# Optimization experiments

Hardware: AMD Instinct MI355X
Metric: run time of the kernel (lower is better)

## Reference

```python
import jax, jax.numpy as jnp
import numpy as np

HEADS = 8
HEIGHT = 512
WIDTH = 512
LATENT = 64  # height // 8
N_INST = 8


def setup_inputs() -> dict:
    key = jax.random.key(0)
    ks = jax.random.split(key, 8)
    C, Cx, L, N = 320, 768, 77, N_INST
    HW = LATENT * LATENT
    hidden_states = jax.random.normal(ks[0], (2, HW, C), jnp.float32)
    encoder_hidden_states = jax.random.normal(ks[1], (N + 3, L, Cx), jnp.float32)
    # non-degenerate normalized boxes (x0, y0, x1, y1)
    rng = np.random.default_rng(0)
    x0 = rng.uniform(0.0, 0.5, (N,)).astype(np.float32)
    y0 = rng.uniform(0.0, 0.5, (N,)).astype(np.float32)
    x1 = (x0 + rng.uniform(0.2, 0.45, (N,))).astype(np.float32)
    y1 = (y0 + rng.uniform(0.2, 0.45, (N,))).astype(np.float32)
    bboxes = jnp.asarray(np.stack([x0, y0, x1, y1], axis=-1)[None], jnp.float32)  # (1, N, 4)
    s = 0.02
    Wq = jax.random.normal(ks[2], (C, C), jnp.float32) * s
    Wk = jax.random.normal(ks[3], (Cx, C), jnp.float32) * s
    Wv = jax.random.normal(ks[4], (Cx, C), jnp.float32) * s
    Wo = jax.random.normal(ks[5], (C, C), jnp.float32) * s
    bo = jnp.zeros((C,), jnp.float32)
    return dict(hidden_states=hidden_states, encoder_hidden_states=encoder_hidden_states,
                bboxes=bboxes, Wq=Wq, Wk=Wk, Wv=Wv, Wo=Wo, bo=bo)


def _heads(x):
    # (B, S, H*D) -> (B*H, S, D)   [diffusers head_to_batch_dim]
    B, S, C = x.shape
    D = C // HEADS
    return x.reshape(B, S, HEADS, D).transpose(0, 2, 1, 3).reshape(B * HEADS, S, D)


def _unheads(x):
    # (B*H, S, D) -> (B, S, H*D)   [diffusers batch_to_head_dim]
    BH, S, D = x.shape
    B = BH // HEADS
    return x.reshape(B, HEADS, S, D).transpose(0, 2, 1, 3).reshape(B, S, HEADS * D)


def _forward(hidden_states, encoder_hidden_states, bboxes, Wq, Wk, Wv, Wo, bo):
    N = bboxes.shape[1]
    HW = hidden_states.shape[1]
    # drop the extra (MIGC) text embedding row, as in the processor
    ehs = encoder_hidden_states[:-1]  # (N+2, L, Cx)
    # batch = [uncond, cond repeated instance_num+1 times]
    hs = jnp.concatenate([hidden_states[:1],
                          jnp.repeat(hidden_states[1:2], N + 1, axis=0)], axis=0)  # (N+2, HW, C)
    q = _heads(hs @ Wq)
    k = _heads(ehs @ Wk)
    v = _heads(ehs @ Wv)
    scale = 1.0 / jnp.sqrt(jnp.asarray(q.shape[-1], q.dtype))
    probs = jax.nn.softmax(jnp.einsum('bqd,bkd->bqk', q, k) * scale, axis=-1)  # ((N+2)*H, HW, L)
    out = _unheads(jnp.einsum('bqk,bkd->bqd', probs, v))  # (N+2, HW, C)
    out = out @ Wo + bo
    hs_uncond = out[:1]
    cond_ca = out[1:][None]  # (1, N+1, HW, C)
    # rasterize per-instance bbox masks at full res (int() truncation == floor for positives)
    b = bboxes[0]  # (N, 4) = x0, y0, x1, y1
    w_min = jnp.floor(WIDTH * b[:, 0])[:, None, None]
    w_max = jnp.floor(WIDTH * b[:, 2])[:, None, None]
    h_min = jnp.floor(HEIGHT * b[:, 1])[:, None, None]
    h_max = jnp.floor(HEIGHT * b[:, 3])[:, None, None]
    rows = jnp.arange(HEIGHT, dtype=jnp.float32)[None, :, None]
    cols = jnp.arange(WIDTH, dtype=jnp.float32)[None, None, :]
    masks = ((rows >= h_min) & (rows < h_max) & (cols >= w_min) & (cols < w_max)).astype(jnp.float32)  # (N,H,W)
    gmask = jax.image.resize(masks, (N, LATENT, LATENT), method='bilinear')  # (N, 64, 64)
    # NaiveFuser: phase weights = [0.1 (full prompt), 10*mask_i], normalized sum over phases
    phase_w = jnp.concatenate([jnp.full((1, HW), 0.1, jnp.float32),
                               gmask.reshape(N, HW) * 10.0], axis=0)  # (N+1, HW)
    w = phase_w[None, :, :, None]  # (1, N+1, HW, 1)
    fused = (cond_ca * w).sum(axis=1) / (w.sum(axis=1) + 1e-6)  # (1, HW, C)
    return jnp.concatenate([hs_uncond, fused], axis=0)  # (2, HW, C)


def reference(hidden_states, encoder_hidden_states, bboxes, Wq, Wk, Wv, Wo, bo):
    return _forward(hidden_states, encoder_hidden_states, bboxes, Wq, Wk, Wv, Wo, bo)
```

## Files before the change

### kernel.cpp

```cpp
#include <hip/hip_runtime.h>
#include <math.h>

#define HW 4096
#define C 320
#define CX 768
#define L 77
#define NB 10
#define NH 8
#define HD 40
#define NINST 8
#define KVC 640
#define SCALE 0.15811388300841898f
#define PSTR 104
#define KSTR 48
#define VSTR 104

typedef _Float16 half8v __attribute__((ext_vector_type(8)));
typedef _Float16 half4v __attribute__((ext_vector_type(4)));
typedef float f32x4 __attribute__((ext_vector_type(4)));

#define KBH (80 * KSTR)
#define VBH (48 * VSTR)

#define SEG_MASK   16
#define N_CVT1     (2 * HW * C / 4)
#define N_CVT2     (NB * L * CX / 4)
#define SEG_CVT    (((N_CVT1 + N_CVT2) + 255) / 256)
#define SEG_WPACK  240
#define SEG_VTZ    195
#define SEG_KPAD   6
#define NPREP      (SEG_MASK + SEG_CVT + SEG_WPACK + SEG_VTZ + SEG_KPAD)

__device__ __forceinline__ float axis_profile(int o, float lo, float hi) {
    float num = 0.f, den = 0.f;
    int j0 = 8 * o - 4;
#pragma unroll
    for (int t = 0; t < 16; ++t) {
        int j = j0 + t;
        float wt = 1.0f - fabsf((float)t - 7.5f) * 0.125f;
        if (j >= 0 && j < 512) {
            den += wt;
            float fj = (float)j;
            if (fj >= lo && fj < hi) num += wt;
        }
    }
    return num / den;
}

__global__ __launch_bounds__(256) void prep_kernel(
        const float* __restrict__ bboxes,
        const float* __restrict__ hs, const float* __restrict__ ehs,
        const float* __restrict__ Wq, const float* __restrict__ Wk,
        const float* __restrict__ Wv, const float* __restrict__ Wo,
        float* __restrict__ wPh, float* __restrict__ wSum,
        _Float16* __restrict__ hsH, _Float16* __restrict__ ehsH,
        _Float16* __restrict__ WqT, _Float16* __restrict__ WkvT,
        _Float16* __restrict__ WoT, _Float16* __restrict__ VTg,
        _Float16* __restrict__ Khp) {
    __shared__ float tile[64][65];
    __shared__ float sw_s[NINST][64];
    __shared__ float sh_s[NINST][4];
    int bx = blockIdx.x, tid = threadIdx.x;

    if (bx < SEG_MASK) {
        int oyb = bx * 4;
        for (int i = tid; i < NINST * 64; i += 256) {
            int n = i >> 6, ox = i & 63;
            float lo = floorf(512.f * bboxes[n * 4 + 0]);
            float hi = floorf(512.f * bboxes[n * 4 + 2]);
            sw_s[n][ox] = axis_profile(ox, lo, hi);
        }
        if (tid < NINST * 4) {
            int n = tid >> 2, oy = tid & 3;
            float lo = floorf(512.f * bboxes[n * 4 + 1]);
            float hi = floorf(512.f * bboxes[n * 4 + 3]);
            sh_s[n][oy] = axis_profile(oyb + oy, lo, hi);
        }
        __syncthreads();
        int oy = tid >> 6, ox = tid & 63;
        int hw = (oyb + oy) * 64 + ox;
        float sum = 0.1f;
        wPh[hw] = 0.1f;
#pragma unroll
        for (int n = 0; n < NINST; ++n) {
            float wv = 10.f * sh_s[n][oy] * sw_s[n][ox];
            wPh[(n + 1) * HW + hw] = wv;
            sum += wv;
        }
        wSum[hw] = sum;
    } else if (bx < SEG_MASK + SEG_CVT) {
        int i = (bx - SEG_MASK) * 256 + tid;
        const float* src; _Float16* dst;
        if (i < N_CVT1) { src = hs; dst = hsH; }
        else if (i < N_CVT1 + N_CVT2) { i -= N_CVT1; src = ehs; dst = ehsH; }
        else return;
        float4 v = ((const float4*)src)[i];
        half4v h = {(_Float16)v.x, (_Float16)v.y, (_Float16)v.z, (_Float16)v.w};
        ((half4v*)dst)[i] = h;
    } else if (bx < SEG_MASK + SEG_CVT + SEG_WPACK) {
        int zz = bx - SEG_MASK - SEG_CVT;
        int z = zz / 60, inner = zz - z * 60;
        int by = inner / 5, bx2 = inner - by * 5;
        const float* W; _Float16* WT; int K;
        if (z == 0)      { W = Wq; WT = WqT; K = C; }
        else if (z == 1) { W = Wk; WT = WkvT; K = CX; }
        else if (z == 2) { W = Wv; WT = WkvT + (size_t)C * CX; K = CX; }
        else             { W = Wo; WT = WoT; K = C; }
        int kt = by * 64;
        if (kt >= K) return;
        int nt = bx2 * 64;
#pragma unroll
        for (int p = 0; p < 16; ++p) {
            int idx = p * 256 + tid;
            int k = idx >> 6, n = idx & 63;
            tile[k][n] = W[(size_t)(kt + k) * C + nt + n];
        }
        __syncthreads();
#pragma unroll
        for (int p = 0; p < 16; ++p) {
            int idx = p * 256 + tid;
            int n = idx >> 6, k = idx & 63;
            WT[(size_t)(nt + n) * K + kt + k] = (_Float16)tile[k][n];
        }
    } else if (bx < SEG_MASK + SEG_CVT + SEG_WPACK + SEG_VTZ) {
        int i = (bx - SEG_MASK - SEG_CVT - SEG_WPACK) * 256 + tid;
        int e0 = i * 8;
        int rem = e0 % VBH;
        int d = rem / VSTR;
        int key0 = rem % VSTR;
        half8v v;
#pragma unroll
        for (int j = 0; j < 8; ++j)
            v[j] = (_Float16)((d == 40 && (key0 + j) < 77) ? 1.f : 0.f);
        ((half8v*)VTg)[i] = v;
    } else {
        int i = (bx - SEG_MASK - SEG_CVT - SEG_WPACK - SEG_VTZ) * 256 + tid;
        if (i < 1440) {
            int rowIdx = i / 6, c8 = i - rowIdx * 6;
            int bh = rowIdx / 3;
            int key = 77 + rowIdx - bh * 3;
            half8v z8 = {(_Float16)0.f,(_Float16)0.f,(_Float16)0.f,(_Float16)0.f,
                         (_Float16)0.f,(_Float16)0.f,(_Float16)0.f,(_Float16)0.f};
            *(half8v*)(Khp + ((size_t)bh * 80 + key) * KSTR + c8 * 8) = z8;
        }
    }
}

__global__ __launch_bounds__(256) void gemm_kv(const _Float16* __restrict__ A,
                                               const _Float16* __restrict__ BT,
                                               _Float16* __restrict__ Khp,
                                               _Float16* __restrict__ VTg) {
    const int K = CX, M = NB * L;
    int lane = threadIdx.x & 63, wave = threadIdx.x >> 6;
    int m0 = blockIdx.y * 64 + wave * 16;
    int n0 = blockIdx.x * 64;
    int lr = lane & 15, kq = (lane >> 4) * 8;
    int arow = m0 + lr; if (arow >= M) arow = M - 1;
    const _Float16* ap = A + (size_t)arow * K + kq;
    const _Float16* bp = BT + (size_t)(n0 + lr) * K + kq;

    half8v afr[24];
#pragma unroll
    for (int i = 0; i < 24; ++i) afr[i] = *(const half8v*)(ap + i * 32);

    f32x4 acc0 = {0.f,0.f,0.f,0.f}, acc1 = acc0, acc2 = acc0, acc3 = acc0;
#pragma unroll
    for (int i = 0; i < 24; ++i) {
        int k0 = i * 32;
        half8v b0 = *(const half8v*)(bp + k0);
        half8v b1 = *(const half8v*)(bp + (size_t)16 * K + k0);
        half8v b2 = *(const half8v*)(bp + (size_t)32 * K + k0);
        half8v b3 = *(const half8v*)(bp + (size_t)48 * K + k0);
        acc0 = __builtin_amdgcn_mfma_f32_16x16x32_f16(afr[i], b0, acc0, 0, 0, 0);
        acc1 = __builtin_amdgcn_mfma_f32_16x16x32_f16(afr[i], b1, acc1, 0, 0, 0);
        acc2 = __builtin_amdgcn_mfma_f32_16x16x32_f16(afr[i], b2, acc2, 0, 0, 0);
        acc3 = __builtin_amdgcn_mfma_f32_16x16x32_f16(afr[i], b3, acc3, 0, 0, 0);
    }
    int rb = m0 + ((lane >> 4) << 2);
    f32x4 accs[4] = {acc0, acc1, acc2, acc3};
#pragma unroll
    for (int t = 0; t < 4; ++t) {
        int col = n0 + t * 16 + lr;
#pragma unroll
        for (int r = 0; r < 4; ++r) {
            int row = rb + r;
            if (row < M) {
                int bb = row / 77;
                int key = row - bb * 77;
                if (col < C) {
                    int h = col / HD, d = col - h * HD;
                    Khp[((size_t)(bb * 8 + h) * 80 + key) * KSTR + d] = (_Float16)accs[t][r];
                } else {
                    int ch = col - C;
                    int h = ch / HD, d = ch - h * HD;
                    VTg[((size_t)(bb * 8 + h) * 48 + d) * VSTR + key] = (_Float16)accs[t][r];
                }
            }
        }
    }
}

__global__ __launch_bounds__(256, 2) void attn_mfma(const _Float16* __restrict__ hsH,
                                                    const _Float16* __restrict__ WqT,
                                                    const _Float16* __restrict__ Khp,
                                                    const _Float16* __restrict__ VTg,
                                                    const float* __restrict__ wPh,
                                                    _Float16* __restrict__ Xh) {
    __shared__ _Float16 smem[2 * (KBH + VBH) + 4 * 2 * 16 * PSTR];
    _Float16* Ks0 = smem;
    _Float16* Vs0 = smem + KBH;
    _Float16* Ks1 = smem + KBH + VBH;
    _Float16* Vs1 = smem + 2 * KBH + VBH;
    _Float16* pbase = smem + 2 * (KBH + VBH);

    int tid = threadIdx.x;
    int wave = tid >> 6, lane = tid & 63;
    int head = blockIdx.x >> 6;
    int qg = blockIdx.x & 63;
    int qrow0 = qg * 64 + wave * 16;
    int c = lane & 15, quad = lane >> 4;
    _Float16* pl0 = pbase + (size_t)(wave * 2) * 16 * PSTR;
    _Float16* pl1 = pl0 + 16 * PSTR;
    half8v zero8 = {(_Float16)0.f,(_Float16)0.f,(_Float16)0.f,(_Float16)0.f,
                    (_Float16)0.f,(_Float16)0.f,(_Float16)0.f,(_Float16)0.f};

    const half8v* Kg8 = (const half8v*)(Khp + (size_t)head * KBH);
    const half8v* Vg8 = (const half8v*)(VTg + (size_t)head * VBH);

    half8v kr0, kr1, vr0, vr1, vr2;
    kr0 = Kg8[tid];
    if (tid < 224) kr1 = Kg8[tid + 256];
    vr0 = Vg8[tid];
    vr1 = Vg8[tid + 256];
    if (tid < 112) vr2 = Vg8[tid + 512];

    float wreg[9];
#pragma unroll
    for (int j = 0; j < 9; ++j)
        wreg[j] = wPh[(size_t)j * HW + qrow0 + c];

#pragma unroll
    for (int i = 0; i < 4; ++i) {
        int idx = i * 64 + lane;
        if (idx < 224) {
            int buf = idx / 112;
            int rem = idx - buf * 112;
            int row = rem / 7, ch = rem - row * 7;
            _Float16* pb = buf ? pl1 : pl0;
            *(half8v*)&pb[row * PSTR + 40 + ch * 8] = zero8;
        }
    }

    {
        const _Float16* bu = hsH + (size_t)(qrow0 + c) * C + quad * 8;
        const _Float16* bc = bu + (size_t)HW * C;
        f32x4 qa0[3] = {}, qa1[3] = {};
        for (int k0 = 0; k0 < C; k0 += 32) {
            half8v hu = *(const half8v*)(bu + k0);
            half8v hc = *(const half8v*)(bc + k0);
#pragma unroll
            for (int t = 0; t < 3; ++t) {
                const _Float16* ap = WqT + (size_t)(head * HD + t * 16 + c) * C + quad * 8 + k0;
                half8v af = *(const half8v*)ap;
                qa0[t] = __builtin_amdgcn_mfma_f32_16x16x32_f16(af, hu, qa0[t], 0, 0, 0);
                qa1[t] = __builtin_amdgcn_mfma_f32_16x16x32_f16(af, hc, qa1[t], 0, 0, 0);
            }
        }
#pragma unroll
        for (int t = 0; t < 3; ++t) {
            if (t < 2 || quad < 2) {
                half4v h0 = {(_Float16)(qa0[t][0] * SCALE), (_Float16)(qa0[t][1] * SCALE),
                             (_Float16)(qa0[t][2] * SCALE), (_Float16)(qa0[t][3] * SCALE)};
                half4v h1 = {(_Float16)(qa1[t][0] * SCALE), (_Float16)(qa1[t][1] * SCALE),
                             (_Float16)(qa1[t][2] * SCALE), (_Float16)(qa1[t][3] * SCALE)};
                *(half4v*)(pl0 + c * PSTR + t * 16 + quad * 4) = h0;
                *(half4v*)(pl1 + c * PSTR + t * 16 + quad * 4) = h1;
            }
        }
    }
    half8v qu0 = *(const half8v*)(pl0 + (size_t)c * PSTR + quad * 8);
    half8v qu1 = *(const half8v*)(pl0 + (size_t)c * PSTR + 32 + quad * 8);
    half8v qc0 = *(const half8v*)(pl1 + (size_t)c * PSTR + quad * 8);
    half8v qc1 = *(const half8v*)(pl1 + (size_t)c * PSTR + 32 + quad * 8);

    {
        half8v* Kd = (half8v*)Ks0;
        half8v* Vd = (half8v*)Vs0;
        Kd[tid] = kr0;
        if (tid < 224) Kd[tid + 256] = kr1;
        Vd[tid] = vr0;
        Vd[tid + 256] = vr1;
        if (tid < 112) Vd[tid + 512] = vr2;
    }
    __syncthreads();

    f32x4 oacc[3] = {};
    int srcl = 32 + c;

    for (int b = 0; b < NB; ++b) {
        if (b + 1 < NB) {
            const half8v* Kn = Kg8 + (size_t)(b + 1) * 8 * (KBH / 8);
            const half8v* Vn = Vg8 + (size_t)(b + 1) * 8 * (VBH / 8);
            kr0 = Kn[tid];
            if (tid < 224) kr1 = Kn[tid + 256];
            vr0 = Vn[tid];
            vr1 = Vn[tid + 256];
            if (tid < 112) vr2 = Vn[tid + 512];
        }

        _Float16* Kb = (b & 1) ? Ks1 : Ks0;
        _Float16* Vb = (b & 1) ? Vs1 : Vs0;
        half8v qb0 = b ? qc0 : qu0;
        half8v qb1 = b ? qc1 : qu1;
        float w = b ? wreg[b - 1] : 1.f;

        f32x4 s[5];
#pragma unroll
        for (int u = 0; u < 5; ++u) {
            half8v ka0 = *(const half8v*)&Kb[(u * 16 + c) * KSTR + quad * 8];
            half8v ka1 = *(const half8v*)&Kb[(u * 16 + c) * KSTR + 32 + quad * 8];
            f32x4 a = {0.f,0.f,0.f,0.f};
            a = __builtin_amdgcn_mfma_f32_16x16x32_f16(ka0, qb0, a, 0, 0, 0);
            a = __builtin_amdgcn_mfma_f32_16x16x32_f16(ka1, qb1, a, 0, 0, 0);
            s[u] = a;
        }

#pragma unroll
        for (int u = 0; u < 5; ++u) {
            half4v h = {(_Float16)__expf(s[u][0]), (_Float16)__expf(s[u][1]),
                        (_Float16)__expf(s[u][2]), (_Float16)__expf(s[u][3])};
            *(half4v*)(pl0 + c * PSTR + u * 16 + quad * 4) = h;
        }
        half8v p0 = *(const half8v*)(pl0 + (size_t)c * PSTR + quad * 8);
        half8v p1 = *(const half8v*)(pl0 + (size_t)c * PSTR + 32 + quad * 8);
        half8v p2 = *(const half8v*)(pl0 + (size_t)c * PSTR + 64 + quad * 8);

        f32x4 ox[3];
#pragma unroll
        for (int t = 0; t < 3; ++t) {
            half8v va0 = *(const half8v*)&Vb[(t * 16 + c) * VSTR + quad * 8];
            half8v va1 = *(const half8v*)&Vb[(t * 16 + c) * VSTR + 32 + quad * 8];
            half8v va2 = *(const half8v*)&Vb[(t * 16 + c) * VSTR + 64 + quad * 8];
            f32x4 a = {0.f,0.f,0.f,0.f};
            a = __builtin_amdgcn_mfma_f32_16x16x32_f16(va0, p0, a, 0, 0, 0);
            a = __builtin_amdgcn_mfma_f32_16x16x32_f16(va1, p1, a, 0, 0, 0);
            a = __builtin_amdgcn_mfma_f32_16x16x32_f16(va2, p2, a, 0, 0, 0);
            ox[t] = a;
        }

        float l = __shfl(ox[2][0], srcl, 64);

        if (b == 0) {
            float rin = 1.0f / l;
#pragma unroll
            for (int t = 0; t < 3; ++t) {
                if (t < 2 || quad < 2) {
                    half4v h = {(_Float16)(ox[t][0] * rin), (_Float16)(ox[t][1] * rin),
                                (_Float16)(ox[t][2] * rin), (_Float16)(ox[t][3] * rin)};
                    *(half4v*)(Xh + (size_t)(qrow0 + c) * C + head * HD + t * 16 + quad * 4) = h;
                }
            }
        } else {
            float rf = w / l;
#pragma unroll
            for (int t = 0; t < 3; ++t) {
                oacc[t][0] += ox[t][0] * rf;
                oacc[t][1] += ox[t][1] * rf;
                oacc[t][2] += ox[t][2] * rf;
                oacc[t][3] += ox[t][3] * rf;
            }
        }

        if (b + 1 < NB) {
            half8v* Kd = (half8v*)((b & 1) ? Ks0 : Ks1);
            half8v* Vd = (half8v*)((b & 1) ? Vs0 : Vs1);
            Kd[tid] = kr0;
            if (tid < 224) Kd[tid + 256] = kr1;
            Vd[tid] = vr0;
            Vd[tid + 256] = vr1;
            if (tid < 112) Vd[tid + 512] = vr2;
        }
        __syncthreads();
    }

#pragma unroll
    for (int t = 0; t < 3; ++t) {
        if (t < 2 || quad < 2) {
            half4v h = {(_Float16)oacc[t][0], (_Float16)oacc[t][1],
                        (_Float16)oacc[t][2], (_Float16)oacc[t][3]};
            *(half4v*)(Xh + (size_t)(HW + qrow0 + c) * C + head * HD + t * 16 + quad * 4) = h;
        }
    }
}

__global__ __launch_bounds__(256, 2) void gemm_oproj_f16(const _Float16* __restrict__ A,
                                                         const _Float16* __restrict__ BT,
                                                         const float* __restrict__ bo,
                                                         const float* __restrict__ wSum,
                                                         float* __restrict__ Out) {
    const int K = C;
    __shared__ _Float16 Bs[64 * 328];
    int tid = threadIdx.x;
    int n0 = blockIdx.x * 64;
    int lane = tid & 63, wave = tid >> 6;
    int m0 = blockIdx.y * 64 + wave * 16;
    int lr = lane & 15, kq = (lane >> 4) * 8;
    const _Float16* ap = A + (size_t)(m0 + lr) * K + kq;

    half8v afr[10];
#pragma unroll
    for (int i = 0; i < 10; ++i) afr[i] = *(const half8v*)(ap + i * 32);

    for (int i = tid; i < 64 * 40; i += 256) {
        int row = i / 40, c8 = i - row * 40;
        *(half8v*)&Bs[row * 328 + c8 * 8] =
            *(const half8v*)(BT + (size_t)(n0 + row) * K + c8 * 8);
    }
    __syncthreads();

    f32x4 acc0 = {0.f,0.f,0.f,0.f}, acc1 = acc0, acc2 = acc0, acc3 = acc0;
#pragma unroll
    for (int i = 0; i < 10; ++i) {
        int k0 = i * 32;
        half8v b0 = *(const half8v*)&Bs[(0 * 16 + lr) * 328 + k0 + kq];
        half8v b1 = *(const half8v*)&Bs[(1 * 16 + lr) * 328 + k0 + kq];
        half8v b2 = *(const half8v*)&Bs[(2 * 16 + lr) * 328 + k0 + kq];
        half8v b3 = *(const half8v*)&Bs[(3 * 16 + lr) * 328 + k0 + kq];
        acc0 = __builtin_amdgcn_mfma_f32_16x16x32_f16(afr[i], b0, acc0, 0, 0, 0);
        acc1 = __builtin_amdgcn_mfma_f32_16x16x32_f16(afr[i], b1, acc1, 0, 0, 0);
        acc2 = __builtin_amdgcn_mfma_f32_16x16x32_f16(afr[i], b2, acc2, 0, 0, 0);
        acc3 = __builtin_amdgcn_mfma_f32_16x16x32_f16(afr[i], b3, acc3, 0, 0, 0);
    }
    int rb = m0 + ((lane >> 4) << 2);
    f32x4 accs[4] = {acc0, acc1, acc2, acc3};
#pragma unroll
    for (int t = 0; t < 4; ++t) {
        int col = n0 + t * 16 + lr;
        float bv = bo[col];
#pragma unroll
        for (int r = 0; r < 4; ++r) {
            int row = rb + r;
            float v = accs[t][r];
            if (row < HW) {
                v += bv;
            } else {
                float ws = wSum[row - HW];
                v = (v + bv * ws) / (ws + 1e-6f);
            }
            Out[(size_t)row * C + col] = v;
        }
    }
}

extern "C" void kernel_launch(void* const* d_in, const int* in_sizes, int n_in,
                              void* d_out, int out_size, void* d_ws, size_t ws_size,
                              hipStream_t stream) {
    const float* hs   = (const float*)d_in[0];
    const float* ehs  = (const float*)d_in[1];
    const float* bbox = (const float*)d_in[2];
    const float* Wq   = (const float*)d_in[3];
    const float* Wk   = (const float*)d_in[4];
    const float* Wv   = (const float*)d_in[5];
    const float* Wo   = (const float*)d_in[6];
    const float* bo   = (const float*)d_in[7];
    float* out = (float*)d_out;

    float* wPh  = (float*)d_ws;
    float* wSum = wPh + (size_t)9 * HW;
    _Float16* hsH  = (_Float16*)(wSum + HW);
    _Float16* ehsH = hsH + (size_t)2 * HW * C;
    _Float16* WqT  = ehsH + (size_t)NB * L * CX;
    _Float16* WkvT = WqT + (size_t)C * C;
    _Float16* WoT  = WkvT + (size_t)KVC * CX;
    _Float16* Khp  = WoT + (size_t)C * C;
    _Float16* VTg  = Khp + (size_t)80 * KBH;
    _Float16* Xh   = VTg + (size_t)80 * VBH;

    prep_kernel<<<dim3(NPREP), 256, 0, stream>>>(bbox, hs, ehs, Wq, Wk, Wv, Wo,
                                                 wPh, wSum, hsH, ehsH, WqT, WkvT, WoT,
                                                 VTg, Khp);
    gemm_kv<<<dim3(KVC / 64, (NB * L + 63) / 64), 256, 0, stream>>>(ehsH, WkvT, Khp, VTg);
    attn_mfma<<<dim3(NH * 64), 256, 0, stream>>>(hsH, WqT, Khp, VTg, wPh, Xh);
    gemm_oproj_f16<<<dim3(C / 64, (2 * HW) / 64), 256, 0, stream>>>(Xh, WoT, bo, wSum, out);
}
```

Baseline: 134.6 us.

## Fuse hidden-state fp16 conversion into attention Q projection and shrink P scratch

Removes the separate fp32-to-fp16 conversion of hidden_states from the prep kernel. The attention kernel now reads fp32 hidden states directly and converts them in registers, which saves a full write and re-read of a 2x4096x320 fp16 buffer. The per-wave P scratch is cut from two buffers to one by staging the uncond and cond Q tiles in sequence, which lowers LDS use. The o-proj GEMM's launch bounds are raised to three blocks per CU. In exchange, each attention block reads twice as many bytes of hidden state, and this is repeated across all 8 heads.

```diff
diff --git a/kernel.cpp b/kernel.cpp
--- a/kernel.cpp
+++ b/kernel.cpp
@@ -23,9 +23,8 @@
 #define VBH (48 * VSTR)
 
 #define SEG_MASK   16
-#define N_CVT1     (2 * HW * C / 4)
 #define N_CVT2     (NB * L * CX / 4)
-#define SEG_CVT    (((N_CVT1 + N_CVT2) + 255) / 256)
+#define SEG_CVT    ((N_CVT2 + 255) / 256)
 #define SEG_WPACK  240
 #define SEG_VTZ    195
 #define SEG_KPAD   6
@@ -49,11 +48,11 @@
 
 __global__ __launch_bounds__(256) void prep_kernel(
         const float* __restrict__ bboxes,
-        const float* __restrict__ hs, const float* __restrict__ ehs,
+        const float* __restrict__ ehs,
         const float* __restrict__ Wq, const float* __restrict__ Wk,
         const float* __restrict__ Wv, const float* __restrict__ Wo,
         float* __restrict__ wPh, float* __restrict__ wSum,
-        _Float16* __restrict__ hsH, _Float16* __restrict__ ehsH,
+        _Float16* __restrict__ ehsH,
         _Float16* __restrict__ WqT, _Float16* __restrict__ WkvT,
         _Float16* __restrict__ WoT, _Float16* __restrict__ VTg,
         _Float16* __restrict__ Khp) {
@@ -90,13 +89,10 @@
         wSum[hw] = sum;
     } else if (bx < SEG_MASK + SEG_CVT) {
         int i = (bx - SEG_MASK) * 256 + tid;
-        const float* src; _Float16* dst;
-        if (i < N_CVT1) { src = hs; dst = hsH; }
-        else if (i < N_CVT1 + N_CVT2) { i -= N_CVT1; src = ehs; dst = ehsH; }
-        else return;
-        float4 v = ((const float4*)src)[i];
+        if (i >= N_CVT2) return;
+        float4 v = ((const float4*)ehs)[i];
         half4v h = {(_Float16)v.x, (_Float16)v.y, (_Float16)v.z, (_Float16)v.w};
-        ((half4v*)dst)[i] = h;
+        ((half4v*)ehsH)[i] = h;
     } else if (bx < SEG_MASK + SEG_CVT + SEG_WPACK) {
         int zz = bx - SEG_MASK - SEG_CVT;
         int z = zz / 60, inner = zz - z * 60;
@@ -200,13 +196,13 @@
     }
 }
 
-__global__ __launch_bounds__(256, 2) void attn_mfma(const _Float16* __restrict__ hsH,
+__global__ __launch_bounds__(256, 2) void attn_mfma(const float* __restrict__ hs,
                                                     const _Float16* __restrict__ WqT,
                                                     const _Float16* __restrict__ Khp,
                                                     const _Float16* __restrict__ VTg,
                                                     const float* __restrict__ wPh,
                                                     _Float16* __restrict__ Xh) {
-    __shared__ _Float16 smem[2 * (KBH + VBH) + 4 * 2 * 16 * PSTR];
+    __shared__ _Float16 smem[2 * (KBH + VBH) + 4 * 16 * PSTR];
     _Float16* Ks0 = smem;
     _Float16* Vs0 = smem + KBH;
     _Float16* Ks1 = smem + KBH + VBH;
@@ -219,8 +215,7 @@
     int qg = blockIdx.x & 63;
     int qrow0 = qg * 64 + wave * 16;
     int c = lane & 15, quad = lane >> 4;
-    _Float16* pl0 = pbase + (size_t)(wave * 2) * 16 * PSTR;
-    _Float16* pl1 = pl0 + 16 * PSTR;
+    _Float16* pl = pbase + (size_t)wave * 16 * PSTR;
     half8v zero8 = {(_Float16)0.f,(_Float16)0.f,(_Float16)0.f,(_Float16)0.f,
                     (_Float16)0.f,(_Float16)0.f,(_Float16)0.f,(_Float16)0.f};
 
@@ -240,24 +235,28 @@
         wreg[j] = wPh[(size_t)j * HW + qrow0 + c];
 
 #pragma unroll
-    for (int i = 0; i < 4; ++i) {
+    for (int i = 0; i < 2; ++i) {
         int idx = i * 64 + lane;
-        if (idx < 224) {
-            int buf = idx / 112;
-            int rem = idx - buf * 112;
-            int row = rem / 7, ch = rem - row * 7;
-            _Float16* pb = buf ? pl1 : pl0;
-            *(half8v*)&pb[row * PSTR + 40 + ch * 8] = zero8;
-        }
-    }
-
+        if (idx < 112) {
+            int row = idx / 7, ch = idx - row * 7;
+            *(half8v*)&pl[row * PSTR + 40 + ch * 8] = zero8;
+        }
+    }
+
+    half8v qu0, qu1, qc0, qc1;
     {
-        const _Float16* bu = hsH + (size_t)(qrow0 + c) * C + quad * 8;
-        const _Float16* bc = bu + (size_t)HW * C;
+        const float* buf = hs + (size_t)(qrow0 + c) * C + quad * 8;
+        const float* bcf = buf + (size_t)HW * C;
         f32x4 qa0[3] = {}, qa1[3] = {};
         for (int k0 = 0; k0 < C; k0 += 32) {
-            half8v hu = *(const half8v*)(bu + k0);
-            half8v hc = *(const half8v*)(bc + k0);
+            float4 u0 = *(const float4*)(buf + k0);
+            float4 u1 = *(const float4*)(buf + k0 + 4);
+            float4 c0 = *(const float4*)(bcf + k0);
+            float4 c1 = *(const float4*)(bcf + k0 + 4);
+            half8v hu = {(_Float16)u0.x, (_Float16)u0.y, (_Float16)u0.z, (_Float16)u0.w,
+                         (_Float16)u1.x, (_Float16)u1.y, (_Float16)u1.z, (_Float16)u1.w};
+            half8v hc = {(_Float16)c0.x, (_Float16)c0.y, (_Float16)c0.z, (_Float16)c0.w,
+                         (_Float16)c1.x, (_Float16)c1.y, (_Float16)c1.z, (_Float16)c1.w};
 #pragma unroll
             for (int t = 0; t < 3; ++t) {
                 const _Float16* ap = WqT + (size_t)(head * HD + t * 16 + c) * C + quad * 8 + k0;
@@ -271,17 +270,22 @@
             if (t < 2 || quad < 2) {
                 half4v h0 = {(_Float16)(qa0[t][0] * SCALE), (_Float16)(qa0[t][1] * SCALE),
                              (_Float16)(qa0[t][2] * SCALE), (_Float16)(qa0[t][3] * SCALE)};
+                *(half4v*)(pl + c * PSTR + t * 16 + quad * 4) = h0;
+            }
+        }
+        qu0 = *(const half8v*)(pl + (size_t)c * PSTR + quad * 8);
+        qu1 = *(const half8v*)(pl + (size_t)c * PSTR + 32 + quad * 8);
+#pragma unroll
+        for (int t = 0; t < 3; ++t) {
+            if (t < 2 || quad < 2) {
                 half4v h1 = {(_Float16)(qa1[t][0] * SCALE), (_Float16)(qa1[t][1] * SCALE),
                              (_Float16)(qa1[t][2] * SCALE), (_Float16)(qa1[t][3] * SCALE)};
-                *(half4v*)(pl0 + c * PSTR + t * 16 + quad * 4) = h0;
-                *(half4v*)(pl1 + c * PSTR + t * 16 + quad * 4) = h1;
-            }
-        }
-    }
-    half8v qu0 = *(const half8v*)(pl0 + (size_t)c * PSTR + quad * 8);
-    half8v qu1 = *(const half8v*)(pl0 + (size_t)c * PSTR + 32 + quad * 8);
-    half8v qc0 = *(const half8v*)(pl1 + (size_t)c * PSTR + quad * 8);
-    half8v qc1 = *(const half8v*)(pl1 + (size_t)c * PSTR + 32 + quad * 8);
+                *(half4v*)(pl + c * PSTR + t * 16 + quad * 4) = h1;
+            }
+        }
+        qc0 = *(const half8v*)(pl + (size_t)c * PSTR + quad * 8);
+        qc1 = *(const half8v*)(pl + (size_t)c * PSTR + 32 + quad * 8);
+    }
 
     {
         half8v* Kd = (half8v*)Ks0;
@@ -329,11 +333,11 @@
         for (int u = 0; u < 5; ++u) {
             half4v h = {(_Float16)__expf(s[u][0]), (_Float16)__expf(s[u][1]),
                         (_Float16)__expf(s[u][2]), (_Float16)__expf(s[u][3])};
-            *(half4v*)(pl0 + c * PSTR + u * 16 + quad * 4) = h;
-        }
-        half8v p0 = *(const half8v*)(pl0 + (size_t)c * PSTR + quad * 8);
-        half8v p1 = *(const half8v*)(pl0 + (size_t)c * PSTR + 32 + quad * 8);
-        half8v p2 = *(const half8v*)(pl0 + (size_t)c * PSTR + 64 + quad * 8);
+            *(half4v*)(pl + c * PSTR + u * 16 + quad * 4) = h;
+        }
+        half8v p0 = *(const half8v*)(pl + (size_t)c * PSTR + quad * 8);
+        half8v p1 = *(const half8v*)(pl + (size_t)c * PSTR + 32 + quad * 8);
+        half8v p2 = *(const half8v*)(pl + (size_t)c * PSTR + 64 + quad * 8);
 
         f32x4 ox[3];
 #pragma unroll
@@ -393,7 +397,7 @@
     }
 }
 
-__global__ __launch_bounds__(256, 2) void gemm_oproj_f16(const _Float16* __restrict__ A,
+__global__ __launch_bounds__(256, 3) void gemm_oproj_f16(const _Float16* __restrict__ A,
                                                          const _Float16* __restrict__ BT,
                                                          const float* __restrict__ bo,
                                                          const float* __restrict__ wSum,
@@ -467,8 +471,7 @@
 
     float* wPh  = (float*)d_ws;
     float* wSum = wPh + (size_t)9 * HW;
-    _Float16* hsH  = (_Float16*)(wSum + HW);
-    _Float16* ehsH = hsH + (size_t)2 * HW * C;
+    _Float16* ehsH = (_Float16*)(wSum + HW);
     _Float16* WqT  = ehsH + (size_t)NB * L * CX;
     _Float16* WkvT = WqT + (size_t)C * C;
     _Float16* WoT  = WkvT + (size_t)KVC * CX;
@@ -476,10 +479,10 @@
     _Float16* VTg  = Khp + (size_t)80 * KBH;
     _Float16* Xh   = VTg + (size_t)80 * VBH;
 
-    prep_kernel<<<dim3(NPREP), 256, 0, stream>>>(bbox, hs, ehs, Wq, Wk, Wv, Wo,
-                                                 wPh, wSum, hsH, ehsH, WqT, WkvT, WoT,
+    prep_kernel<<<dim3(NPREP), 256, 0, stream>>>(bbox, ehs, Wq, Wk, Wv, Wo,
+                                                 wPh, wSum, ehsH, WqT, WkvT, WoT,
                                                  VTg, Khp);
     gemm_kv<<<dim3(KVC / 64, (NB * L + 63) / 64), 256, 0, stream>>>(ehsH, WkvT, Khp, VTg);
-    attn_mfma<<<dim3(NH * 64), 256, 0, stream>>>(hsH, WqT, Khp, VTg, wPh, Xh);
+    attn_mfma<<<dim3(NH * 64), 256, 0, stream>>>(hs, WqT, Khp, VTg, wPh, Xh);
     gemm_oproj_f16<<<dim3(C / 64, (2 * HW) / 64), 256, 0, stream>>>(Xh, WoT, bo, wSum, out);
 }
```

New measurement: 136.4 us. Within noise of the previous version (+1.3%).
